# Kernel tuning notes

Measured on AMD Instinct MI355X. Metric: run time of the kernel, lower is better.

Reference implementation:

```python
import jax, jax.numpy as jnp
import numpy as np
from jax import lax

IMG_SIZE = 640
STRIDES = (8, 16, 32)
NA = 3          # anchors per level
NC = 80         # classes
CONF_THRESH = 0.001
NMS_THRESH = 0.6
ANCHORS = np.array([[10,13],[16,30],[33,23],[30,61],[62,45],[59,119],[116,90],[156,198],[373,326]], np.float32).reshape(3, 3, 2)

def _make_grids():
    gs, st, aw = [], [], []
    for i, s in enumerate(STRIDES):
        hs = ws = IMG_SIZE // s
        gy, gx = np.meshgrid(np.arange(hs), np.arange(ws), indexing='ij')
        gxy = np.stack([gx, gy], -1).astype(np.float32).reshape(1, hs*ws, 1, 2)
        gs.append(gxy)
        st.append(np.full((1, hs*ws, NA, 2), s, np.float32))
        aw.append(np.tile(ANCHORS[i][None], (hs*ws, 1, 1)))
    return (np.concatenate(gs, 1), np.concatenate(st, 1), np.concatenate(aw, 0)[None])

GRID_CELL, STRIDE_T, ANCH_WH = _make_grids()  # [1,HW,1,2], [1,HW,3,2], [1,HW,3,2]

def _nms_classaware(boxes, score, valid):
    # Greedy NMS, class-aware via coordinate offset already applied to boxes.
    # Faithful to the numpy baseline: w,h = max(1e-28, .), areas without +1.
    x1, y1, x2, y2 = boxes[:, 0], boxes[:, 1], boxes[:, 2], boxes[:, 3]
    areas = (x2 - x1) * (y2 - y1)
    order = jnp.argsort(-score)
    N = boxes.shape[0]
    def body(i, state):
        supp, keep = state
        idx = order[i]
        active = jnp.logical_and(jnp.logical_not(supp[idx]), valid[idx])
        keep = keep.at[idx].set(active)
        xx1 = jnp.maximum(x1[idx], x1)
        yy1 = jnp.maximum(y1[idx], y1)
        xx2 = jnp.minimum(x2[idx], x2)
        yy2 = jnp.minimum(y2[idx], y2)
        w = jnp.maximum(1e-28, xx2 - xx1)
        h = jnp.maximum(1e-28, yy2 - yy1)
        inter = w * h
        iou = inter / (areas[idx] + areas - inter)
        newsupp = jnp.logical_and(iou > NMS_THRESH, active)
        newsupp = newsupp.at[idx].set(False)
        return jnp.logical_or(supp, newsupp), keep
    supp0 = jnp.zeros((N,), bool)
    keep0 = jnp.zeros((N,), bool)
    _, keep = lax.fori_loop(0, N, body, (supp0, keep0))
    return keep

def _decode_and_nms(pred_s, pred_m, pred_l):
    objs, clss, regs = [], [], []
    for pred in (pred_s, pred_m, pred_l):
        B, C, H, W = pred.shape
        p = pred.transpose(0, 2, 3, 1).reshape(B, H*W, C)
        objs.append(p[..., :NA].reshape(B, H*W*NA, 1))
        clss.append(p[..., NA:NA*(1+NC)].reshape(B, H*W*NA, NC))
        regs.append(p[..., NA*(1+NC):].reshape(B, H*W, NA, 4))
    obj_pred = jnp.concatenate(objs, axis=1)   # [B, N, 1]
    cls_pred = jnp.concatenate(clss, axis=1)   # [B, N, NC]
    reg_pred = jnp.concatenate(regs, axis=1)   # [B, HW, 3, 4]
    grid = jnp.asarray(GRID_CELL)
    stride = jnp.asarray(STRIDE_T)
    anch = jnp.asarray(ANCH_WH)
    B = reg_pred.shape[0]
    c_xy = (jax.nn.sigmoid(reg_pred[..., :2]) + grid) * stride
    b_wh = jnp.exp(reg_pred[..., 2:]) * anch
    xywh = jnp.concatenate([c_xy, b_wh], -1).reshape(B, -1, 4)
    x1y1 = xywh[..., :2] - xywh[..., 2:] / 2
    x2y2 = xywh[..., :2] + xywh[..., 2:] / 2
    boxes = jnp.clip(jnp.concatenate([x1y1, x2y2], -1) / IMG_SIZE, 0.0, 1.0)[0]  # [N,4]
    obj_s = jax.nn.sigmoid(obj_pred)[0]                     # [N,1]
    scores_all = jax.nn.softmax(cls_pred[0], axis=1) * obj_s  # [N,NC]
    cls_ind = jnp.argmax(scores_all, axis=1)                # [N]
    score = jnp.max(scores_all, axis=1)                     # [N]
    valid = score >= CONF_THRESH
    # class-aware NMS: offset normalized boxes by 2*class so classes never overlap
    boxes_off = boxes + cls_ind[:, None].astype(boxes.dtype) * 2.0
    keep = _nms_classaware(lax.stop_gradient(boxes_off), lax.stop_gradient(score), valid)
    out = jnp.concatenate([
        boxes,                                    # 4 cols
        score[:, None],                           # 1 col
        cls_ind[:, None].astype(boxes.dtype),     # 1 col (non-diff)
        keep[:, None].astype(boxes.dtype),        # 1 col (non-diff)
    ], axis=1)                                    # [N, 7]
    return out

def setup_inputs() -> dict:
    key = jax.random.key(0)
    k1, k2, k3 = jax.random.split(key, 3)
    return {
        'pred_s': jax.random.normal(k1, (1, 255, 80, 80), jnp.float32),
        'pred_m': jax.random.normal(k2, (1, 255, 40, 40), jnp.float32),
        'pred_l': jax.random.normal(k3, (1, 255, 20, 20), jnp.float32),
    }

def reference(pred_s, pred_m, pred_l):
    return _decode_and_nms(pred_s, pred_m, pred_l)
```

## Files before the change

### kernel.cpp

```cpp
#include <hip/hip_runtime.h>
#include <cstdint>

#define NPRED 25200
#define NPOS  8400
#define NCLS  80
#define CAP   512
#define CSTRIDE 16
#define MW    8
#define NCHUNK 132

__device__ __forceinline__ float sigmoidf_(float x) { return 1.0f / (1.0f + expf(-x)); }

__global__ __launch_bounds__(64) void decode_kernel(
    const float* __restrict__ ps, const float* __restrict__ pm, const float* __restrict__ pl,
    float* __restrict__ out, int* __restrict__ counts,
    float4* __restrict__ g_boxin, uint64_t* __restrict__ g_key)
{
    int chunk = blockIdx.x;
    int a     = blockIdx.y;
    int t     = threadIdx.x;

    const float* p; int HW, W, base, si; float stride; int w0;
    if (chunk < 100)      { p = ps; HW = 6400; W = 80; stride = 8.f;  base = 0;    si = 0; w0 = chunk * 64; }
    else if (chunk < 125) { p = pm; HW = 1600; W = 40; stride = 16.f; base = 6400; si = 1; w0 = (chunk - 100) * 64; }
    else                  { p = pl; HW = 400;  W = 20; stride = 32.f; base = 8000; si = 2; w0 = (chunk - 125) * 64; }

    int local = w0 + t;
    bool valid = local < HW;
    int lclamp = valid ? local : (HW - 1);

    __shared__ float lds[NCLS * 64];

    const float* cbase = p + (size_t)(3 + a * NCLS) * HW;
    int lane_c = t >> 4;
    int j      = (t & 15) << 2;
    int off    = w0 + j; if (off > HW - 4) off = HW - 4;

    float4 vreg[20];
#pragma unroll
    for (int r0 = 0; r0 < 20; r0++)
        vreg[r0] = *(const float4*)(cbase + (size_t)(r0 * 4 + lane_c) * HW + off);
    float objl = p[(size_t)a * HW + lclamp];
    const float* rb = p + (size_t)(3 + 3 * NCLS + a * 4) * HW + lclamp;
    float tx = rb[0], ty = rb[(size_t)HW], tw = rb[(size_t)2 * HW], th = rb[(size_t)3 * HW];
#pragma unroll
    for (int r0 = 0; r0 < 20; r0++)
        *(float4*)&lds[(r0 * 4 + lane_c) * 64 + j] = vreg[r0];
    __syncthreads();

    float m = -INFINITY;
#pragma unroll 16
    for (int c = 0; c < NCLS; c++) m = fmaxf(m, lds[c * 64 + t]);
    float s = 0.f;
#pragma unroll 16
    for (int c = 0; c < NCLS; c++) {
        float e = expf(lds[c * 64 + t] - m);
        lds[c * 64 + t] = e;
        s += e;
    }
    float obj = sigmoidf_(objl);
    float best = -1.f; int bi = 0;
#pragma unroll 16
    for (int c = 0; c < NCLS; c++) {
        float sc = lds[c * 64 + t] / s * obj;
        if (sc > best) { best = sc; bi = c; }
    }

    if (!valid) return;

    const float AW[9] = {10.f,16.f,33.f, 30.f,62.f,59.f, 116.f,156.f,373.f};
    const float AH[9] = {13.f,30.f,23.f, 61.f,45.f,119.f, 90.f,198.f,326.f};
    float aw = AW[si*3 + a], ah = AH[si*3 + a];

    int y = local / W;
    int x = local - y * W;
    float cx = (sigmoidf_(tx) + (float)x) * stride;
    float cy = (sigmoidf_(ty) + (float)y) * stride;
    float bw = expf(tw) * aw;
    float bh = expf(th) * ah;
    float x1 = fminf(fmaxf((cx - bw / 2.f) / 640.f, 0.f), 1.f);
    float y1 = fminf(fmaxf((cy - bh / 2.f) / 640.f, 0.f), 1.f);
    float x2 = fminf(fmaxf((cx + bw / 2.f) / 640.f, 0.f), 1.f);
    float y2 = fminf(fmaxf((cy + bh / 2.f) / 640.f, 0.f), 1.f);

    int g = (base + local) * 3 + a;
    float clsf = (float)bi;
    float* o = out + (size_t)g * 7;
    o[0] = x1; o[1] = y1; o[2] = x2; o[3] = y2;
    o[4] = best; o[5] = clsf; o[6] = 0.f;

    if (best >= 0.001f) {
        int slot = atomicAdd(&counts[bi * CSTRIDE], 1);
        if (slot < CAP) {
            float off2 = clsf * 2.0f;
            g_boxin[bi * CAP + slot] = make_float4(x1 + off2, y1 + off2,
                                                   x2 + off2, y2 + off2);
            unsigned u = __float_as_uint(best);
            u = (u & 0x80000000u) ? ~u : (u | 0x80000000u);
            g_key[bi * CAP + slot] = ((uint64_t)(~u) << 15) | (uint64_t)g;
        }
    }
}

__global__ __launch_bounds__(256) void nms_sort_kernel(
    const int* __restrict__ counts, const uint64_t* __restrict__ g_key,
    const float4* __restrict__ g_boxin, float4* __restrict__ g_sbox,
    int* __restrict__ g_sg)
{
    int c  = blockIdx.x;
    int i0 = blockIdx.y << 6;
    int n = counts[c * CSTRIDE]; if (n > CAP) n = CAP;
    if (i0 >= n) return;
    int tid = threadIdx.x;

    __shared__ uint64_t key[CAP];
    for (int i = tid; i < n; i += 256) key[i] = g_key[c * CAP + i];
    __syncthreads();

    int item = i0 + (tid >> 2);
    int sub  = tid & 3;
    bool act = item < n;
    int r = 0;
    uint64_t k = 0;
    if (act) {
        k = key[item];
        int nq = (n + 3) >> 2;
        int lo = sub * nq; if (lo > n) lo = n;
        int hi = lo + nq;  if (hi > n) hi = n;
        int jj = lo;
        for (; jj + 8 <= hi; jj += 8) {
            int t0 = key[jj]   < k, t1 = key[jj+1] < k;
            int t2 = key[jj+2] < k, t3 = key[jj+3] < k;
            int t4 = key[jj+4] < k, t5 = key[jj+5] < k;
            int t6 = key[jj+6] < k, t7 = key[jj+7] < k;
            r += t0 + t1 + t2 + t3 + t4 + t5 + t6 + t7;
        }
        for (; jj < hi; jj++) r += (key[jj] < k);
    }
    r += __shfl_xor(r, 1);
    r += __shfl_xor(r, 2);
    if (act && sub == 0) {
        g_sbox[c * CAP + r] = g_boxin[c * CAP + item];
        g_sg[c * CAP + r] = (int)(k & 0x7FFF);
    }
}

__global__ __launch_bounds__(256) void nms_build_kernel(
    const int* __restrict__ counts, const float4* __restrict__ g_sbox,
    uint64_t* __restrict__ g_mask)
{
    int c = blockIdx.x;
    int w = blockIdx.y;
    int n = counts[c * CSTRIDE]; if (n > CAP) n = CAP;
    int j0 = w << 6;
    if (j0 >= n) return;
    int j1 = j0 + 64; if (j1 > n) j1 = n;
    int cnt = j1 - j0;
    int tid = threadIdx.x;

    __shared__ float4 sb[64];
    if (tid < 64) {
        float4 sv = make_float4(3e30f, 3e30f, 3e30f, 3e30f);
        if (tid < cnt) sv = g_sbox[c * CAP + j0 + tid];
        sb[tid] = sv;
    }
    __syncthreads();

    uint64_t* gm = g_mask + (size_t)c * MW * CAP + (size_t)w * CAP;
    for (int i = tid; i < n; i += 256) {
        float4 b4 = g_sbox[c * CAP + i];
        float Ai = (b4.z - b4.x) * (b4.w - b4.y);
        uint64_t bits = 0;
        if (i + 1 < j1) {
#pragma unroll 8
            for (int jq = 0; jq < 64; jq++) {
                float4 bj = sb[jq];
                float xx1 = fmaxf(b4.x, bj.x);
                float yy1 = fmaxf(b4.y, bj.y);
                float xx2 = fminf(b4.z, bj.z);
                float yy2 = fminf(b4.w, bj.w);
                float ww = fmaxf(1e-28f, xx2 - xx1);
                float hh = fmaxf(1e-28f, yy2 - yy1);
                float inter = ww * hh;
                float Aj = (bj.z - bj.x) * (bj.w - bj.y);
                float iou = inter / ((Ai + Aj) - inter);
                if ((j0 + jq) > i && iou > 0.6f) bits |= 1ull << jq;
            }
        }
        gm[i] = bits;
    }
}

__global__ __launch_bounds__(64) void nms_scan_kernel(
    const int* __restrict__ counts, const int* __restrict__ g_sg,
    const uint64_t* __restrict__ g_mask, float* __restrict__ out)
{
    int c = blockIdx.x;
    int n = counts[c * CSTRIDE]; if (n > CAP) n = CAP;
    int nw = (n + 63) >> 6;
    int lane = threadIdx.x;

    const uint64_t* gm = g_mask + (size_t)c * MW * CAP;
    const int* sg = g_sg + c * CAP;

    uint64_t removed = 0;
    for (int w = 0; w < nw; w++) {
        uint64_t rw = __shfl(removed, w);
        int row = (w << 6) + lane;
        uint64_t diag = (row < n) ? gm[w * CAP + row] : 0ull;
        int rem = n - (w << 6);
        uint64_t valid = (rem >= 64) ? ~0ull : ((1ull << rem) - 1ull);
        uint64_t nulls = __ballot(diag == 0ull);
        uint64_t cand = ~rw & valid;
        uint64_t kw = 0;
        uint64_t it = cand & ~nulls;
        while (it) {
            int b = __ffsll((unsigned long long)it) - 1;
            kw |= 1ull << b;
            uint64_t db = __shfl(diag, b);
            it &= ~db; cand &= ~db;
            it &= ~(1ull << b);
        }
        kw |= cand & nulls;

        int g  = lane >> 3;
        int wp = lane & 7;
        uint64_t acc = 0;
        if (wp < nw) {
            uint64_t mybits = kw & (0xFFull << (g * 8));
            while (mybits) {
                int b = __ffsll((unsigned long long)mybits) - 1;
                mybits &= mybits - 1;
                acc |= gm[wp * CAP + ((w << 6) + b)];
            }
        }
        acc |= __shfl_xor(acc, 8);
        acc |= __shfl_xor(acc, 16);
        acc |= __shfl_xor(acc, 32);
        if (lane < MW) removed |= acc;

        if (row < n && ((kw >> lane) & 1))
            out[(size_t)sg[row] * 7 + 6] = 1.0f;
    }
}

extern "C" void kernel_launch(void* const* d_in, const int* in_sizes, int n_in,
                              void* d_out, int out_size, void* d_ws, size_t ws_size,
                              hipStream_t stream) {
    const float* ps = (const float*)d_in[0];
    const float* pm = (const float*)d_in[1];
    const float* pl = (const float*)d_in[2];
    float* out = (float*)d_out;

    char* ws = (char*)d_ws;
    int*      counts  = (int*)ws;
    float4*   g_boxin = (float4*)(ws + 8192);
    uint64_t* g_key   = (uint64_t*)(ws + 663552);
    float4*   g_sbox  = (float4*)(ws + 991232);
    int*      g_sg    = (int*)(ws + 1646592);
    uint64_t* g_mask  = (uint64_t*)(ws + 1810432);

    hipMemsetAsync(counts, 0, 8192, stream);
    decode_kernel<<<dim3(NCHUNK, 3), 64, 0, stream>>>(ps, pm, pl, out, counts, g_boxin, g_key);
    nms_sort_kernel<<<dim3(NCLS, MW), 256, 0, stream>>>(counts, g_key, g_boxin, g_sbox, g_sg);
    nms_build_kernel<<<dim3(NCLS, MW), 256, 0, stream>>>(counts, g_sbox, g_mask);
    nms_scan_kernel<<<NCLS, 64, 0, stream>>>(counts, g_sg, g_mask, out);
}
```

Before: 111.5 us.

## Fuse NMS sort, mask build and scan into one per-class kernel using LDS

Merges the three per-class NMS kernels into a single block per class. Keys, boxes, sorted boxes and the suppression mask are kept in shared memory instead of round-tripping through global workspace. The scan also skips mask words below the diagonal. This removes two kernel launches and global traffic, but each class now runs on one 256-thread block, with less parallelism and high LDS usage.

```diff
diff --git a/kernel.cpp b/kernel.cpp
--- a/kernel.cpp
+++ b/kernel.cpp
@@ -102,79 +102,69 @@
     }
 }
 
-__global__ __launch_bounds__(256) void nms_sort_kernel(
+__global__ __launch_bounds__(256) void nms_fused_kernel(
     const int* __restrict__ counts, const uint64_t* __restrict__ g_key,
-    const float4* __restrict__ g_boxin, float4* __restrict__ g_sbox,
-    int* __restrict__ g_sg)
-{
-    int c  = blockIdx.x;
-    int i0 = blockIdx.y << 6;
-    int n = counts[c * CSTRIDE]; if (n > CAP) n = CAP;
-    if (i0 >= n) return;
-    int tid = threadIdx.x;
-
-    __shared__ uint64_t key[CAP];
-    for (int i = tid; i < n; i += 256) key[i] = g_key[c * CAP + i];
-    __syncthreads();
-
-    int item = i0 + (tid >> 2);
-    int sub  = tid & 3;
-    bool act = item < n;
-    int r = 0;
-    uint64_t k = 0;
-    if (act) {
-        k = key[item];
-        int nq = (n + 3) >> 2;
-        int lo = sub * nq; if (lo > n) lo = n;
-        int hi = lo + nq;  if (hi > n) hi = n;
-        int jj = lo;
-        for (; jj + 8 <= hi; jj += 8) {
-            int t0 = key[jj]   < k, t1 = key[jj+1] < k;
-            int t2 = key[jj+2] < k, t3 = key[jj+3] < k;
-            int t4 = key[jj+4] < k, t5 = key[jj+5] < k;
-            int t6 = key[jj+6] < k, t7 = key[jj+7] < k;
-            r += t0 + t1 + t2 + t3 + t4 + t5 + t6 + t7;
-        }
-        for (; jj < hi; jj++) r += (key[jj] < k);
-    }
-    r += __shfl_xor(r, 1);
-    r += __shfl_xor(r, 2);
-    if (act && sub == 0) {
-        g_sbox[c * CAP + r] = g_boxin[c * CAP + item];
-        g_sg[c * CAP + r] = (int)(k & 0x7FFF);
-    }
-}
-
-__global__ __launch_bounds__(256) void nms_build_kernel(
-    const int* __restrict__ counts, const float4* __restrict__ g_sbox,
-    uint64_t* __restrict__ g_mask)
+    const float4* __restrict__ g_boxin, float* __restrict__ out)
 {
     int c = blockIdx.x;
-    int w = blockIdx.y;
     int n = counts[c * CSTRIDE]; if (n > CAP) n = CAP;
-    int j0 = w << 6;
-    if (j0 >= n) return;
-    int j1 = j0 + 64; if (j1 > n) j1 = n;
-    int cnt = j1 - j0;
+    if (n == 0) return;
     int tid = threadIdx.x;
-
-    __shared__ float4 sb[64];
-    if (tid < 64) {
-        float4 sv = make_float4(3e30f, 3e30f, 3e30f, 3e30f);
-        if (tid < cnt) sv = g_sbox[c * CAP + j0 + tid];
-        sb[tid] = sv;
-    }
-    __syncthreads();
-
-    uint64_t* gm = g_mask + (size_t)c * MW * CAP + (size_t)w * CAP;
+    int nw = (n + 63) >> 6;
+
+    __shared__ uint64_t key_s[CAP];
+    __shared__ float4   boxu_s[CAP];
+    __shared__ float4   sbox_s[CAP + 64];
+    __shared__ int      sg_s[CAP];
+    __shared__ uint64_t mask_s[MW * CAP];
+
     for (int i = tid; i < n; i += 256) {
-        float4 b4 = g_sbox[c * CAP + i];
+        key_s[i]  = g_key[c * CAP + i];
+        boxu_s[i] = g_boxin[c * CAP + i];
+    }
+    for (int i = n + tid; i < n + 64; i += 256)
+        sbox_s[i] = make_float4(3e30f, 3e30f, 3e30f, 3e30f);
+    __syncthreads();
+
+    for (int i0 = 0; i0 < n; i0 += 64) {
+        int item = i0 + (tid >> 2);
+        int sub  = tid & 3;
+        bool act = item < n;
+        int r = 0;
+        uint64_t k = 0;
+        if (act) {
+            k = key_s[item];
+            int nq = (n + 3) >> 2;
+            int lo = sub * nq; if (lo > n) lo = n;
+            int hi = lo + nq;  if (hi > n) hi = n;
+            int jj = lo;
+            for (; jj + 8 <= hi; jj += 8) {
+                int t0 = key_s[jj]   < k, t1 = key_s[jj+1] < k;
+                int t2 = key_s[jj+2] < k, t3 = key_s[jj+3] < k;
+                int t4 = key_s[jj+4] < k, t5 = key_s[jj+5] < k;
+                int t6 = key_s[jj+6] < k, t7 = key_s[jj+7] < k;
+                r += t0 + t1 + t2 + t3 + t4 + t5 + t6 + t7;
+            }
+            for (; jj < hi; jj++) r += (key_s[jj] < k);
+        }
+        r += __shfl_xor(r, 1);
+        r += __shfl_xor(r, 2);
+        if (act && sub == 0) {
+            sbox_s[r] = boxu_s[item];
+            sg_s[r]   = (int)(k & 0x7FFF);
+        }
+    }
+    __syncthreads();
+
+    for (int i = tid; i < n; i += 256) {
+        float4 b4 = sbox_s[i];
         float Ai = (b4.z - b4.x) * (b4.w - b4.y);
-        uint64_t bits = 0;
-        if (i + 1 < j1) {
+        for (int w = i >> 6; w < nw; w++) {
+            int j0 = w << 6;
+            uint64_t bits = 0;
 #pragma unroll 8
             for (int jq = 0; jq < 64; jq++) {
-                float4 bj = sb[jq];
+                float4 bj = sbox_s[j0 + jq];
                 float xx1 = fmaxf(b4.x, bj.x);
                 float yy1 = fmaxf(b4.y, bj.y);
                 float xx2 = fminf(b4.z, bj.z);
@@ -186,28 +176,18 @@
                 float iou = inter / ((Ai + Aj) - inter);
                 if ((j0 + jq) > i && iou > 0.6f) bits |= 1ull << jq;
             }
-        }
-        gm[i] = bits;
-    }
-}
-
-__global__ __launch_bounds__(64) void nms_scan_kernel(
-    const int* __restrict__ counts, const int* __restrict__ g_sg,
-    const uint64_t* __restrict__ g_mask, float* __restrict__ out)
-{
-    int c = blockIdx.x;
-    int n = counts[c * CSTRIDE]; if (n > CAP) n = CAP;
-    int nw = (n + 63) >> 6;
-    int lane = threadIdx.x;
-
-    const uint64_t* gm = g_mask + (size_t)c * MW * CAP;
-    const int* sg = g_sg + c * CAP;
-
+            mask_s[w * CAP + i] = bits;
+        }
+    }
+    __syncthreads();
+
+    if (tid >= 64) return;
+    int lane = tid;
     uint64_t removed = 0;
     for (int w = 0; w < nw; w++) {
         uint64_t rw = __shfl(removed, w);
         int row = (w << 6) + lane;
-        uint64_t diag = (row < n) ? gm[w * CAP + row] : 0ull;
+        uint64_t diag = (row < n) ? mask_s[w * CAP + row] : 0ull;
         int rem = n - (w << 6);
         uint64_t valid = (rem >= 64) ? ~0ull : ((1ull << rem) - 1ull);
         uint64_t nulls = __ballot(diag == 0ull);
@@ -226,12 +206,12 @@
         int g  = lane >> 3;
         int wp = lane & 7;
         uint64_t acc = 0;
-        if (wp < nw) {
+        if (wp >= w && wp < nw) {
             uint64_t mybits = kw & (0xFFull << (g * 8));
             while (mybits) {
                 int b = __ffsll((unsigned long long)mybits) - 1;
                 mybits &= mybits - 1;
-                acc |= gm[wp * CAP + ((w << 6) + b)];
+                acc |= mask_s[wp * CAP + ((w << 6) + b)];
             }
         }
         acc |= __shfl_xor(acc, 8);
@@ -240,7 +220,7 @@
         if (lane < MW) removed |= acc;
 
         if (row < n && ((kw >> lane) & 1))
-            out[(size_t)sg[row] * 7 + 6] = 1.0f;
+            out[(size_t)sg_s[row] * 7 + 6] = 1.0f;
     }
 }
 
@@ -256,13 +236,8 @@
     int*      counts  = (int*)ws;
     float4*   g_boxin = (float4*)(ws + 8192);
     uint64_t* g_key   = (uint64_t*)(ws + 663552);
-    float4*   g_sbox  = (float4*)(ws + 991232);
-    int*      g_sg    = (int*)(ws + 1646592);
-    uint64_t* g_mask  = (uint64_t*)(ws + 1810432);
 
     hipMemsetAsync(counts, 0, 8192, stream);
     decode_kernel<<<dim3(NCHUNK, 3), 64, 0, stream>>>(ps, pm, pl, out, counts, g_boxin, g_key);
-    nms_sort_kernel<<<dim3(NCLS, MW), 256, 0, stream>>>(counts, g_key, g_boxin, g_sbox, g_sg);
-    nms_build_kernel<<<dim3(NCLS, MW), 256, 0, stream>>>(counts, g_sbox, g_mask);
-    nms_scan_kernel<<<NCLS, 64, 0, stream>>>(counts, g_sg, g_mask, out);
+    nms_fused_kernel<<<NCLS, 256, 0, stream>>>(counts, g_key, g_boxin, out);
 }
```

Result: slower. 136.1 us (+22.1%).
